# Kernel tuning notes

Measured on AMD Instinct MI355X. Metric: run time of the kernel, lower is better.

## Reference

```python
import jax, jax.numpy as jnp
import numpy as np

SCALE = 1.0  # std of the Normal error model (init arg `scale`)
B, P, D, T = 32, 256, 64, 4096


def setup_inputs() -> dict:
    key = jax.random.key(0)
    k1, k2, k3 = jax.random.split(key, 3)
    data = jax.random.normal(k1, (B, P, D), dtype=jnp.float32)
    targets = jax.random.normal(k2, (B, P), dtype=jnp.float32)
    task_pool = jax.random.normal(k3, (T, D, 1), dtype=jnp.float32)
    return {"data": data, "targets": targets, "task_pool": task_pool}


def reference(data, targets, task_pool):
    # W: (n_dims, n_tasks), matching task_pool.squeeze(-1).T in the original
    W = task_pool[..., 0].T
    dt = data.dtype

    # Per-point, per-task predictions and Gaussian log-likelihoods, computed ONCE.
    # The original recomputes X@W and the log-prob sum for every prefix i (O(n^2));
    # here a single cumsum over the point axis reproduces the same prefix sums.
    pred_per_task = jnp.einsum('bpd,dt->bpt', data, W)          # (B, P, T)
    err = targets[..., None] - pred_per_task                     # (B, P, T)
    log_norm = -jnp.log(jnp.asarray(SCALE, dt)) - 0.5 * jnp.log(jnp.asarray(2.0 * np.pi, dt))
    scores = -0.5 * (err / SCALE) ** 2 + log_norm                # Normal(0, scale).log_prob

    cum = jnp.cumsum(scores, axis=1)                             # cum[:, i] = sum_{j<=i}
    # Posterior for predicting point i uses points 0..i-1; point 0 uses a uniform
    # posterior (original: W.mean(dim=1) == softmax(zeros) @ W.T).
    log_lik = jnp.concatenate([jnp.zeros_like(cum[:, :1]), cum[:, :-1]], axis=1)
    post = jax.nn.softmax(log_lik, axis=-1)                      # (B, P, T)

    w_mmse = jnp.einsum('bpt,dt->bpd', post, W)                  # posterior-mean weights
    return jnp.einsum('bpd,bpd->bp', data, w_mmse)               # (B, P)
```

## Files before the change

### kernel.cpp

```cpp
#include <hip/hip_runtime.h>
#include <hip/hip_bf16.h>
#include <math.h>

#define Bb 32
#define Pp 256
#define Dd 64
#define Tt 4096

typedef unsigned short ushort_t;
typedef __attribute__((ext_vector_type(8))) short bf16x8;
typedef __attribute__((ext_vector_type(4))) float f32x4;

#define TRIP_BYTES ((size_t)Bb * Pp * 64 * 8)
#define WS_NEED    TRIP_BYTES

#define C2 (-0.7213475204444817f)

__device__ __forceinline__ float fexp2(float x) {
  float r; asm("v_exp_f32 %0, %1" : "=v"(r) : "v"(x)); return r;
}
__device__ __forceinline__ float flog2(float x) {
  float r; asm("v_log_f32 %0, %1" : "=v"(r) : "v"(x)); return r;
}
__device__ __forceinline__ float frcp(float x) {
  float r; asm("v_rcp_f32 %0, %1" : "=v"(r) : "v"(x)); return r;
}

template <int CTRL>
__device__ __forceinline__ float dppf(float x) {
  return __builtin_bit_cast(float,
      __builtin_amdgcn_update_dpp(0, __builtin_bit_cast(int, x), CTRL, 0xF, 0xF, true));
}

__device__ __forceinline__ f32x4 mfma6(bf16x8 ah0, bf16x8 ah1, bf16x8 al0, bf16x8 al1,
                                       bf16x8 bh0, bf16x8 bh1, bf16x8 bl0, bf16x8 bl1) {
  f32x4 a = (f32x4)0.f;
  a = __builtin_amdgcn_mfma_f32_16x16x32_bf16(ah0, bh0, a, 0, 0, 0);
  a = __builtin_amdgcn_mfma_f32_16x16x32_bf16(ah1, bh1, a, 0, 0, 0);
  a = __builtin_amdgcn_mfma_f32_16x16x32_bf16(ah0, bl0, a, 0, 0, 0);
  a = __builtin_amdgcn_mfma_f32_16x16x32_bf16(al0, bh0, a, 0, 0, 0);
  a = __builtin_amdgcn_mfma_f32_16x16x32_bf16(ah1, bl1, a, 0, 0, 0);
  a = __builtin_amdgcn_mfma_f32_16x16x32_bf16(al1, bh1, a, 0, 0, 0);
  return a;
}

__device__ __forceinline__ void cvt8(const float4 a, const float4 b,
                                     bf16x8& hi, bf16x8& lo) {
#define CVT1(X, IDX)                                          \
  {                                                           \
    const __hip_bfloat16 hb = __float2bfloat16(X);            \
    const float hf = __bfloat162float(hb);                    \
    const __hip_bfloat16 lb = __float2bfloat16((X) - hf);     \
    hi[IDX] = __builtin_bit_cast(short, hb);                  \
    lo[IDX] = __builtin_bit_cast(short, lb);                  \
  }
  CVT1(a.x, 0) CVT1(a.y, 1) CVT1(a.z, 2) CVT1(a.w, 3)
  CVT1(b.x, 4) CVT1(b.y, 5) CVT1(b.z, 6) CVT1(b.w, 7)
#undef CVT1
}

__global__ __launch_bounds__(256, 2) void k_main(const float* __restrict__ data,
                                                 const float* __restrict__ targets,
                                                 const float* __restrict__ task_pool,
                                                 float2* __restrict__ trips) {
  const int tid  = threadIdx.x;
  const int wid  = tid >> 6;
  const int lane = tid & 63;
  const int quad = lane >> 4;
  const int l16  = lane & 15;
  const int b     = blockIdx.x >> 4;
  const int strip = blockIdx.x & 15;
  const int t0    = strip * 256;
  const int wstrip = strip * 4 + wid;

  bf16x8 vbh0[4], vbh1[4], vbl0[4], vbl1[4];
#pragma unroll
  for (int nt = 0; nt < 4; ++nt) {
    const float* wr = task_pool + (size_t)(t0 + wid * 64 + nt * 16 + l16) * Dd + quad * 8;
    cvt8(*(const float4*)(wr),      *(const float4*)(wr + 4),  vbh0[nt], vbl0[nt]);
    cvt8(*(const float4*)(wr + 32), *(const float4*)(wr + 36), vbh1[nt], vbl1[nt]);
  }

  const float* arow = data + (size_t)b * Pp * Dd;
  const float* tgt  = targets + b * Pp;
  float2* __restrict__ trb = trips + (size_t)b * Pp * 64;

  float R[4];
#pragma unroll
  for (int nt = 0; nt < 4; ++nt) R[nt] = 0.f;

  bf16x8 ah0, ah1, al0, al1;
  {
    const float* ar = arow + (size_t)l16 * Dd + quad * 8;
    cvt8(*(const float4*)(ar),      *(const float4*)(ar + 4),  ah0, al0);
    cvt8(*(const float4*)(ar + 32), *(const float4*)(ar + 36), ah1, al1);
  }
  float4 tq = *(const float4*)(tgt + quad * 4);

#pragma unroll 1
  for (int sg = 0; sg < 16; ++sg) {
    const int pn = ((sg + 1) & 15) * 16;
    const float* an = arow + (size_t)(pn + l16) * Dd + quad * 8;
    const float4 nf0 = *(const float4*)(an);
    const float4 nf1 = *(const float4*)(an + 4);
    const float4 nf2 = *(const float4*)(an + 32);
    const float4 nf3 = *(const float4*)(an + 36);
    const float4 ntq = *(const float4*)(tgt + pn + quad * 4);

    float cc[4][4], av[4][4];
#pragma unroll
    for (int nt = 0; nt < 4; ++nt) {
      const f32x4 a = mfma6(ah0, ah1, al0, al1,
                            vbh0[nt], vbh1[nt], vbl0[nt], vbl1[nt]);
      float sc0, sc1, sc2, sc3;
      { const float e = tq.x - a[0]; sc0 = C2 * e * e; }
      { const float e = tq.y - a[1]; sc1 = C2 * e * e; }
      { const float e = tq.z - a[2]; sc2 = C2 * e * e; }
      { const float e = tq.w - a[3]; sc3 = C2 * e * e; }

      const float colsum = (sc0 + sc1) + (sc2 + sc3);
      const float x1 = __shfl_xor(colsum, 16, 64);
      const float x2 = __shfl_xor(colsum, 32, 64);
      const float x3 = __shfl_xor(x1, 32, 64);
      const float pre = (quad == 0) ? 0.f
                      : (quad == 1) ? x1
                      : (quad == 2) ? (x2 + x3)
                                    : (x1 + x2 + x3);
      const float base = R[nt] + pre;
      cc[nt][0] = base;
      cc[nt][1] = base + sc0;
      cc[nt][2] = cc[nt][1] + sc1;
      cc[nt][3] = cc[nt][2] + sc2;
      av[nt][0] = a[0]; av[nt][1] = a[1]; av[nt][2] = a[2]; av[nt][3] = a[3];
      R[nt] += ((colsum + x1) + (x2 + x3));
    }

    float M[4];
#pragma unroll
    for (int r = 0; r < 4; ++r)
      M[r] = fmaxf(fmaxf(cc[0][r], cc[1][r]), fmaxf(cc[2][r], cc[3][r]));
#pragma unroll
    for (int r = 0; r < 4; ++r) M[r] = fmaxf(M[r], dppf<0xB1>(M[r]));
#pragma unroll
    for (int r = 0; r < 4; ++r) M[r] = fmaxf(M[r], dppf<0x4E>(M[r]));
#pragma unroll
    for (int r = 0; r < 4; ++r) M[r] = fmaxf(M[r], dppf<0x141>(M[r]));
#pragma unroll
    for (int r = 0; r < 4; ++r) M[r] = fmaxf(M[r], dppf<0x140>(M[r]));

    float ss[4], vv[4];
#pragma unroll
    for (int r = 0; r < 4; ++r) {
      float s = 0.f, v = 0.f;
#pragma unroll
      for (int nt = 0; nt < 4; ++nt) {
        const float e = fexp2(cc[nt][r] - M[r]);
        s += e;
        v = fmaf(e, av[nt][r], v);
      }
      ss[r] = s; vv[r] = v;
    }

#pragma unroll
    for (int r = 0; r < 4; ++r) { ss[r] += dppf<0xB1>(ss[r]);  vv[r] += dppf<0xB1>(vv[r]); }
#pragma unroll
    for (int r = 0; r < 4; ++r) { ss[r] += dppf<0x4E>(ss[r]);  vv[r] += dppf<0x4E>(vv[r]); }
#pragma unroll
    for (int r = 0; r < 4; ++r) { ss[r] += dppf<0x141>(ss[r]); vv[r] += dppf<0x141>(vv[r]); }
#pragma unroll
    for (int r = 0; r < 4; ++r) { ss[r] += dppf<0x140>(ss[r]); vv[r] += dppf<0x140>(vv[r]); }

    if (l16 == 0) {
#pragma unroll
      for (int r = 0; r < 4; ++r) {
        const float lm = M[r] + flog2(ss[r]);
        const float u  = vv[r] * frcp(ss[r]);
        const int p = sg * 16 + quad * 4 + r;
        trb[p * 64 + wstrip] = make_float2(lm, u);
      }
    }

    cvt8(nf0, nf1, ah0, al0);
    cvt8(nf2, nf3, ah1, al1);
    tq = ntq;
  }
}

__global__ __launch_bounds__(256) void k_merge(const float2* __restrict__ ws,
                                               float* __restrict__ out) {
  const int gt   = blockIdx.x * 256 + threadIdx.x;
  const int bp   = gt >> 6;
  const int lane = gt & 63;
  const float2 e = ws[(size_t)bp * 64 + lane];
  float M = e.x;
#pragma unroll
  for (int off = 32; off; off >>= 1) M = fmaxf(M, __shfl_xor(M, off, 64));
  const float f = fexp2(e.x - M);
  float S = f, V = f * e.y;
#pragma unroll
  for (int off = 32; off; off >>= 1) {
    S += __shfl_xor(S, off, 64);
    V += __shfl_xor(V, off, 64);
  }
  if (lane == 0) out[bp] = V / S;
}

__global__ __launch_bounds__(256) void k_scan_fused(const float* __restrict__ data,
                                                    const float* __restrict__ targets,
                                                    const float* __restrict__ task_pool,
                                                    float2* __restrict__ ws) {
  const int b     = blockIdx.x >> 4;
  const int wid   = threadIdx.x >> 6;
  const int lane  = threadIdx.x & 63;
  const int chunk = ((blockIdx.x & 15) << 2) | wid;
  const int t     = (chunk << 6) | lane;
  float w[Dd];
#pragma unroll
  for (int d = 0; d < Dd; d += 4) {
    const float4 r = *(const float4*)(task_pool + (size_t)t * Dd + d);
    w[d] = r.x; w[d + 1] = r.y; w[d + 2] = r.z; w[d + 3] = r.w;
  }
  const float* drow = data + (size_t)b * (Pp * Dd);
  const float* tgt  = targets + b * Pp;
  float2* wsb       = ws + (size_t)b * (Pp * 64);
  float c = 0.f;
  for (int p = 0; p < Pp; ++p) {
    float a0 = 0.f, a1 = 0.f, a2 = 0.f, a3 = 0.f;
    const float* r = drow + p * Dd;
#pragma unroll
    for (int d = 0; d < Dd; d += 4) {
      a0 = fmaf(r[d], w[d], a0);         a1 = fmaf(r[d + 1], w[d + 1], a1);
      a2 = fmaf(r[d + 2], w[d + 2], a2); a3 = fmaf(r[d + 3], w[d + 3], a3);
    }
    const float pred = (a0 + a1) + (a2 + a3);
    float m = c;
#pragma unroll
    for (int off = 32; off; off >>= 1) m = fmaxf(m, __shfl_xor(m, off, 64));
    const float e = fexp2(c - m);
    float s = e, v = e * pred;
#pragma unroll
    for (int off = 32; off; off >>= 1) {
      s += __shfl_xor(s, off, 64);
      v += __shfl_xor(v, off, 64);
    }
    if (lane == 0) wsb[p * 64 + chunk] = make_float2(m + flog2(s), v * frcp(s));
    const float err = tgt[p] - pred;
    c = fmaf(C2 * err, err, c);
  }
}

extern "C" void kernel_launch(void* const* d_in, const int* in_sizes, int n_in,
                              void* d_out, int out_size, void* d_ws, size_t ws_size,
                              hipStream_t stream) {
  const float* data      = (const float*)d_in[0];
  const float* targets   = (const float*)d_in[1];
  const float* task_pool = (const float*)d_in[2];
  float* out = (float*)d_out;

  float2* trips = (float2*)d_ws;
  if (ws_size >= WS_NEED) {
    k_main <<<dim3(Bb * 16), dim3(256), 0, stream>>>(data, targets, task_pool, trips);
    k_merge<<<dim3((Bb * Pp * 64) / 256), dim3(256), 0, stream>>>(trips, out);
  } else {
    k_scan_fused<<<dim3(512), dim3(256), 0, stream>>>(data, targets, task_pool, trips);
    k_merge<<<dim3((Bb * Pp * 64) / 256), dim3(256), 0, stream>>>(trips, out);
  }
}
```

Before: 97.20 us.

## Split each point scan across two blocks with a cheap prefix-recompute phase

Doubles the grid so each (batch, task strip) is handled by two blocks. The second block first recomputes only the running column sums for the first SPLIT point groups, then does the full softmax work for the rest. The split point is chosen to balance the two halves. This raises parallelism from 512 to 1024 blocks and allows 4 blocks per CU via launch bounds, at the cost of redundant MFMA work and removal of the next-tile software prefetch of data.

Measured after the change: 114.7 us. 18.0% more time.

```diff
diff --git a/kernel.cpp b/kernel.cpp
--- a/kernel.cpp
+++ b/kernel.cpp
@@ -59,7 +59,8 @@
 #undef CVT1
 }
 
-__global__ __launch_bounds__(256, 2) void k_main(const float* __restrict__ data,
+#define SPLIT 10
+__global__ __launch_bounds__(256, 4) void k_main(const float* __restrict__ data,
                                                  const float* __restrict__ targets,
                                                  const float* __restrict__ task_pool,
                                                  float2* __restrict__ trips) {
@@ -68,8 +69,9 @@
   const int lane = tid & 63;
   const int quad = lane >> 4;
   const int l16  = lane & 15;
-  const int b     = blockIdx.x >> 4;
-  const int strip = blockIdx.x & 15;
+  const int b     = blockIdx.x >> 5;
+  const int strip = (blockIdx.x >> 1) & 15;
+  const int half  = blockIdx.x & 1;
   const int t0    = strip * 256;
   const int wstrip = strip * 4 + wid;
 
@@ -89,23 +91,41 @@
 #pragma unroll
   for (int nt = 0; nt < 4; ++nt) R[nt] = 0.f;
 
-  bf16x8 ah0, ah1, al0, al1;
-  {
-    const float* ar = arow + (size_t)l16 * Dd + quad * 8;
+  if (half) {
+#pragma unroll 1
+    for (int sg = 0; sg < SPLIT; ++sg) {
+      const float* ar = arow + (size_t)(sg * 16 + l16) * Dd + quad * 8;
+      bf16x8 ah0, ah1, al0, al1;
+      cvt8(*(const float4*)(ar),      *(const float4*)(ar + 4),  ah0, al0);
+      cvt8(*(const float4*)(ar + 32), *(const float4*)(ar + 36), ah1, al1);
+      const float4 tq = *(const float4*)(tgt + sg * 16 + quad * 4);
+#pragma unroll
+      for (int nt = 0; nt < 4; ++nt) {
+        const f32x4 a = mfma6(ah0, ah1, al0, al1,
+                              vbh0[nt], vbh1[nt], vbl0[nt], vbl1[nt]);
+        float sc0, sc1, sc2, sc3;
+        { const float e = tq.x - a[0]; sc0 = C2 * e * e; }
+        { const float e = tq.y - a[1]; sc1 = C2 * e * e; }
+        { const float e = tq.z - a[2]; sc2 = C2 * e * e; }
+        { const float e = tq.w - a[3]; sc3 = C2 * e * e; }
+        const float colsum = (sc0 + sc1) + (sc2 + sc3);
+        const float x1 = __shfl_xor(colsum, 16, 64);
+        const float x2 = __shfl_xor(colsum, 32, 64);
+        const float x3 = __shfl_xor(x1, 32, 64);
+        R[nt] += ((colsum + x1) + (x2 + x3));
+      }
+    }
+  }
+
+  const int fullBeg = half ? SPLIT : 0;
+  const int fullEnd = half ? 16 : SPLIT;
+#pragma unroll 1
+  for (int sg = fullBeg; sg < fullEnd; ++sg) {
+    const float* ar = arow + (size_t)(sg * 16 + l16) * Dd + quad * 8;
+    bf16x8 ah0, ah1, al0, al1;
     cvt8(*(const float4*)(ar),      *(const float4*)(ar + 4),  ah0, al0);
     cvt8(*(const float4*)(ar + 32), *(const float4*)(ar + 36), ah1, al1);
-  }
-  float4 tq = *(const float4*)(tgt + quad * 4);
-
-#pragma unroll 1
-  for (int sg = 0; sg < 16; ++sg) {
-    const int pn = ((sg + 1) & 15) * 16;
-    const float* an = arow + (size_t)(pn + l16) * Dd + quad * 8;
-    const float4 nf0 = *(const float4*)(an);
-    const float4 nf1 = *(const float4*)(an + 4);
-    const float4 nf2 = *(const float4*)(an + 32);
-    const float4 nf3 = *(const float4*)(an + 36);
-    const float4 ntq = *(const float4*)(tgt + pn + quad * 4);
+    const float4 tq = *(const float4*)(tgt + sg * 16 + quad * 4);
 
     float cc[4][4], av[4][4];
 #pragma unroll
@@ -179,10 +199,6 @@
         trb[p * 64 + wstrip] = make_float2(lm, u);
       }
     }
-
-    cvt8(nf0, nf1, ah0, al0);
-    cvt8(nf2, nf3, ah1, al1);
-    tq = ntq;
   }
 }
 
@@ -259,7 +275,7 @@
 
   float2* trips = (float2*)d_ws;
   if (ws_size >= WS_NEED) {
-    k_main <<<dim3(Bb * 16), dim3(256), 0, stream>>>(data, targets, task_pool, trips);
+    k_main <<<dim3(Bb * 32), dim3(256), 0, stream>>>(data, targets, task_pool, trips);
     k_merge<<<dim3((Bb * Pp * 64) / 256), dim3(256), 0, stream>>>(trips, out);
   } else {
     k_scan_fused<<<dim3(512), dim3(256), 0, stream>>>(data, targets, task_pool, trips);
```
